# Optimization experiments

Measured on AMD Instinct MI355X. Metric: run time of the kernel, lower is better.

The kernel has to match this reference:

```python
import jax, jax.numpy as jnp
import numpy as np

N_NODES = 50000
N_RELS = 8
IN_DIM = 128
OUT_DIM = 128
N_EDGES = 800000


def setup_inputs() -> dict:
    key = jax.random.key(0)
    k1, k2, k3, k4 = jax.random.split(key, 4)
    src = jax.random.randint(k1, (N_EDGES,), 0, N_NODES, dtype=jnp.int64 if jax.config.jax_enable_x64 else jnp.int32)
    rel = jax.random.randint(k2, (N_EDGES,), 0, N_RELS, dtype=src.dtype)
    tgt = jax.random.randint(k3, (N_EDGES,), 0, N_NODES, dtype=src.dtype)
    triples = jnp.stack([src, rel, tgt], axis=1)  # (E, 3) like torch layout (s, r, t)
    features = jax.random.normal(k4, (N_NODES, IN_DIM), dtype=jnp.float32)
    weights = jax.random.normal(jax.random.fold_in(key, 1), (N_RELS, IN_DIM, OUT_DIM), dtype=jnp.float32) * (1.0 / np.sqrt(IN_DIM))
    bias = jnp.zeros((OUT_DIM,), dtype=jnp.float32)
    return {"triples": triples, "features": features, "weights": weights, "bias": bias}


def reference(triples, features, weights, bias):
    # RGCN-NC forward, horizontal stacking (featured mode):
    #   out[t] = sum_{(s,r,t) in E} (1/c_{t,r}) * features[s] @ W[r] + bias
    # where c_{t,r} = #edges sharing the same (relation, target) pair,
    # matching sum_sparse(..., row_normalisation=False) on the (n x r*n) adjacency.
    src, rel, tgt = triples[:, 0], triples[:, 1], triples[:, 2]
    n = features.shape[0]
    r = weights.shape[0]
    e = triples.shape[0]

    # per-(rel, tgt) edge counts -> 1/c normalization per edge
    key = rel * n + tgt  # column index of horizontally stacked adjacency
    counts = jax.ops.segment_sum(jnp.ones((e,), dtype=features.dtype), key, num_segments=r * n)
    vals = 1.0 / counts[key]  # (E,)

    # dense per-relation transform: H[r] = X @ W[r]   (r, n, out)
    h = jnp.einsum('ni,rio->rno', features, weights)

    # gather per-edge messages, scale, scatter-add into targets
    msgs = h[rel, src] * vals[:, None]  # (E, out)
    out = jax.ops.segment_sum(msgs, tgt, num_segments=n)  # (n, out)
    return out + bias
```

## Files before the change

### kernel.cpp

```cpp
#include <hip/hip_runtime.h>
#include <hip/hip_bf16.h>

#define N_NODES 50000
#define N_RELS 8
#define IN_DIM 128
#define OUT_DIM 128
#define N_EDGES 800000
#define NR (N_NODES * N_RELS)
#define KDIM (N_RELS * IN_DIM)
#define SCAN_ELEMS 2048
#define SCAN_NBLK ((NR + SCAN_ELEMS - 1) / SCAN_ELEMS)
#define M_PAD 50048
#define CNT_BLKS ((N_EDGES / 4 + 255) / 256)
#define CW_BLKS ((N_RELS * IN_DIM * OUT_DIM + 255) / 256)
#define FB_BLKS ((N_NODES * IN_DIM / 8 + 255) / 256)

typedef __attribute__((ext_vector_type(8))) short bf16x8;
typedef __attribute__((ext_vector_type(4))) float floatx4;
typedef __attribute__((ext_vector_type(4))) unsigned int uintx4;

__device__ inline unsigned short f2bf(float f) {
    unsigned u = __builtin_bit_cast(unsigned, f);
    u += 0x7fff + ((u >> 16) & 1);
    return (unsigned short)(u >> 16);
}
__device__ inline float bflo(unsigned u) {
    return __builtin_bit_cast(float, u << 16);
}
__device__ inline float bfhi(unsigned u) {
    return __builtin_bit_cast(float, u & 0xffff0000u);
}

__global__ void prep_kernel(const int* __restrict__ tri, const float* __restrict__ W,
                            const float* __restrict__ features,
                            int* __restrict__ cnt, unsigned short* __restrict__ Wtf,
                            unsigned short* __restrict__ featB) {
    const int b = blockIdx.x;
    if (b < CNT_BLKS) {
        int t = b * 256 + threadIdx.x;
        if (t >= N_EDGES / 4) return;
        const int4* tri4 = (const int4*)tri;
        int4 a = tri4[3 * t], v = tri4[3 * t + 1], c = tri4[3 * t + 2];
        atomicAdd(&cnt[a.z * N_RELS + a.y], 1);
        atomicAdd(&cnt[v.y * N_RELS + v.x], 1);
        atomicAdd(&cnt[c.x * N_RELS + v.w], 1);
        atomicAdd(&cnt[c.w * N_RELS + c.z], 1);
    } else if (b < CNT_BLKS + CW_BLKS) {
        int idx = (b - CNT_BLKS) * 256 + threadIdx.x;
        if (idx >= N_RELS * IN_DIM * OUT_DIM) return;
        int e  = idx & 7;
        int l  = (idx >> 3) & 63;
        int ks = (idx >> 9) & 31;
        int nt = idx >> 14;
        int o = nt * 16 + (l & 15);
        int k = ks * 32 + (l >> 4) * 8 + e;
        Wtf[idx] = f2bf(W[(k >> 7) * (IN_DIM * OUT_DIM) + (k & 127) * OUT_DIM + o]);
    } else {
        int t = (b - CNT_BLKS - CW_BLKS) * 256 + threadIdx.x;
        if (t >= N_NODES * IN_DIM / 8) return;
        const float4* f4 = (const float4*)features;
        float4 x = f4[2 * t], y = f4[2 * t + 1];
        uint4 o;
        o.x = (unsigned)f2bf(x.x) | ((unsigned)f2bf(x.y) << 16);
        o.y = (unsigned)f2bf(x.z) | ((unsigned)f2bf(x.w) << 16);
        o.z = (unsigned)f2bf(y.x) | ((unsigned)f2bf(y.y) << 16);
        o.w = (unsigned)f2bf(y.z) | ((unsigned)f2bf(y.w) << 16);
        ((uint4*)featB)[t] = o;
    }
}

__global__ void scan_part(const int* __restrict__ cnt, int* __restrict__ bsum) {
    __shared__ int s[256];
    int b = blockIdx.x, t = threadIdx.x;
    int base = b * SCAN_ELEMS + t * 8;
    int sum = 0;
#pragma unroll
    for (int k = 0; k < 8; ++k) {
        int i = base + k;
        sum += (i < NR) ? cnt[i] : 0;
    }
    s[t] = sum; __syncthreads();
    for (int off = 128; off > 0; off >>= 1) {
        if (t < off) s[t] += s[t + off];
        __syncthreads();
    }
    if (t == 0) bsum[b] = s[0];
}

__global__ __launch_bounds__(256) void scan_fused(
    const int* __restrict__ cnt, const int* __restrict__ bsum,
    int* __restrict__ segOff, int* __restrict__ cursor)
{
    __shared__ int s[256];
    __shared__ int sboff;
    const int b = blockIdx.x, t = threadIdx.x;

    int vb = (t < SCAN_NBLK) ? bsum[t] : 0;
    s[t] = vb; __syncthreads();
    for (int off = 1; off < 256; off <<= 1) {
        int x = (t >= off) ? s[t - off] : 0;
        __syncthreads();
        s[t] += x;
        __syncthreads();
    }
    if (t == 0) sboff = (b == 0) ? 0 : s[b - 1];
    __syncthreads();
    const int boff = sboff;

    const int base = b * SCAN_ELEMS + t * 8;
    int v[8]; int sum = 0;
#pragma unroll
    for (int k = 0; k < 8; ++k) {
        int i = base + k;
        v[k] = (i < NR) ? cnt[i] : 0;
        sum += v[k];
    }
    s[t] = sum; __syncthreads();
    for (int off = 1; off < 256; off <<= 1) {
        int x = (t >= off) ? s[t - off] : 0;
        __syncthreads();
        s[t] += x;
        __syncthreads();
    }
    int run = boff + s[t] - sum;
#pragma unroll
    for (int k = 0; k < 8; ++k) {
        int i = base + k;
        if (i < NR) { segOff[i] = run; cursor[i] = run; run += v[k]; }
    }
    if (b == 0 && t == 0) segOff[NR] = N_EDGES;
}

__global__ void scatter_kernel(const int* __restrict__ tri, int* __restrict__ cursor,
                               int* __restrict__ sortedSrc) {
    int e = blockIdx.x * 256 + threadIdx.x;
    if (e >= N_EDGES) return;
    int src = tri[3 * e];
    int rel = tri[3 * e + 1];
    int tgt = tri[3 * e + 2];
    int p = atomicAdd(&cursor[tgt * N_RELS + rel], 1);
    sortedSrc[p] = src;
}

__global__ __launch_bounds__(256) void agg_kernel(
    const int* __restrict__ sortedSrc, const int* __restrict__ segOff,
    const unsigned short* __restrict__ featB, unsigned short* __restrict__ aggG)
{
    const int wave = threadIdx.x >> 6, lane = threadIdx.x & 63;
    const int node = blockIdx.x * 4 + wave;
    const int q = lane >> 4, l16 = lane & 15;

    int bnd = 0;
    if (lane < 9) bnd = segOff[node * N_RELS + lane];
    int s[9];
#pragma unroll
    for (int i = 0; i < 9; ++i) s[i] = __shfl(bnd, i);

    const int e0 = s[0], eN = s[8];
    int srcw = 0;
    if (e0 + lane < eN) srcw = sortedSrc[e0 + lane];

    const unsigned short* fb = featB + 8 * l16;
    unsigned short* dst = aggG + (size_t)node * KDIM + 8 * l16;

#pragma unroll
    for (int p = 0; p < 2; ++p) {
        const int r = 4 * p + q;
        const int s0v = s[r], s1v = s[r + 1];
        const int len = s1v - s0v;
        int m0x = __shfl_xor(len, 16);
        int jm = (len > m0x) ? len : m0x;
        int m1x = __shfl_xor(jm, 32);
        const int jmax = (jm > m1x) ? jm : m1x;
        float a0 = 0.f, a1 = 0.f, a2 = 0.f, a3 = 0.f;
        float a4 = 0.f, a5 = 0.f, a6 = 0.f, a7 = 0.f;
        for (int j = 0; j < jmax; j += 2) {
            const int ea = s0v + j;
            const int ia = ea - e0;
            const int swina = __shfl(srcw, ia & 63);
            const int eb = ea + 1;
            const int ib = ia + 1;
            const int swinb = __shfl(srcw, ib & 63);
            const bool pa = j < len;
            const bool pb = j + 1 < len;
            int srca = 0, srcb = 0;
            if (pa) srca = (ia < 64) ? swina : sortedSrc[ea];
            if (pb) srcb = (ib < 64) ? swinb : sortedSrc[eb];
            uint4 ua = *(const uint4*)&fb[srca * IN_DIM];
            uint4 ub = *(const uint4*)&fb[srcb * IN_DIM];
            if (pa) {
                a0 += bflo(ua.x); a1 += bfhi(ua.x);
                a2 += bflo(ua.y); a3 += bfhi(ua.y);
                a4 += bflo(ua.z); a5 += bfhi(ua.z);
                a6 += bflo(ua.w); a7 += bfhi(ua.w);
            }
            if (pb) {
                a0 += bflo(ub.x); a1 += bfhi(ub.x);
                a2 += bflo(ub.y); a3 += bfhi(ub.y);
                a4 += bflo(ub.z); a5 += bfhi(ub.z);
                a6 += bflo(ub.w); a7 += bfhi(ub.w);
            }
        }
        const float inv = (len > 0) ? 1.0f / (float)len : 0.0f;
        uintx4 pk;
        pk[0] = (unsigned)f2bf(a0 * inv) | ((unsigned)f2bf(a1 * inv) << 16);
        pk[1] = (unsigned)f2bf(a2 * inv) | ((unsigned)f2bf(a3 * inv) << 16);
        pk[2] = (unsigned)f2bf(a4 * inv) | ((unsigned)f2bf(a5 * inv) << 16);
        pk[3] = (unsigned)f2bf(a6 * inv) | ((unsigned)f2bf(a7 * inv) << 16);
        __builtin_nontemporal_store(pk, (uintx4*)&dst[r * IN_DIM]);
    }
}

__global__ __launch_bounds__(256) void gemm_kernel(
    const unsigned short* __restrict__ aggG,
    const unsigned short* __restrict__ Wtf,
    const float* __restrict__ bias,
    float* __restrict__ out)
{
    __shared__ unsigned short Abuf[64 * 128];
    const int tid = threadIdx.x;
    const int wave = tid >> 6, lane = tid & 63;
    const int qk = lane >> 4, ln16 = lane & 15;
    const int m0 = blockIdx.x * 64;
    const int wm = wave & 1, wn = wave >> 1;

    floatx4 acc[2][4];
#pragma unroll
    for (int st = 0; st < 2; ++st)
#pragma unroll
        for (int nt = 0; nt < 4; ++nt) acc[st][nt] = (floatx4){0.f, 0.f, 0.f, 0.f};

    const int l4 = lane >> 4, l15 = lane & 15;

    for (int c = 0; c < 8; ++c) {
        __syncthreads();
#pragma unroll
        for (int i = 0; i < 4; ++i) {
            const int row = wave * 16 + i * 4 + l4;
            const int unit = l15 ^ (row & 15);
            const unsigned short* g =
                aggG + (size_t)(m0 + row) * KDIM + c * 128 + unit * 8;
            __builtin_amdgcn_global_load_lds(
                (const __attribute__((address_space(1))) unsigned int*)g,
                (__attribute__((address_space(3))) unsigned int*)&Abuf[(wave * 16 + i * 4) * 128],
                16, 0, 0);
        }
        __syncthreads();

#pragma unroll
        for (int ksl = 0; ksl < 4; ++ksl) {
            const int ks = c * 4 + ksl;
            bf16x8 a[2];
#pragma unroll
            for (int st = 0; st < 2; ++st) {
                const int r = wm * 32 + st * 16 + ln16;
                const int u = (ksl * 4 + qk) ^ (r & 15);
                a[st] = *(const bf16x8*)&Abuf[r * 128 + u * 8];
            }
#pragma unroll
            for (int nt = 0; nt < 4; ++nt) {
                const int ntg = wn * 4 + nt;
                bf16x8 b = *(const bf16x8*)&Wtf[(size_t)((ntg * 32 + ks) * 64 + lane) * 8];
                acc[0][nt] = __builtin_amdgcn_mfma_f32_16x16x32_bf16(a[0], b, acc[0][nt], 0, 0, 0);
                acc[1][nt] = __builtin_amdgcn_mfma_f32_16x16x32_bf16(a[1], b, acc[1][nt], 0, 0, 0);
            }
        }
    }

#pragma unroll
    for (int nt = 0; nt < 4; ++nt) {
        const int o = (wn * 4 + nt) * 16 + ln16;
        const float bv = bias[o];
#pragma unroll
        for (int st = 0; st < 2; ++st)
#pragma unroll
            for (int j = 0; j < 4; ++j) {
                const int t = m0 + wm * 32 + st * 16 + qk * 4 + j;
                if (t < N_NODES) out[(size_t)t * OUT_DIM + o] = acc[st][nt][j] + bv;
            }
    }
}

extern "C" void kernel_launch(void* const* d_in, const int* in_sizes, int n_in,
                              void* d_out, int out_size, void* d_ws, size_t ws_size,
                              hipStream_t stream)
{
    const int*   tri      = (const int*)d_in[0];
    const float* features = (const float*)d_in[1];
    const float* W        = (const float*)d_in[2];
    const float* bias     = (const float*)d_in[3];
    float* out = (float*)d_out;

    char* ws = (char*)d_ws;
    unsigned short* Wtf = (unsigned short*)ws; ws += (size_t)OUT_DIM * KDIM * 2;
    int* cnt       = (int*)ws; ws += (size_t)NR * 4;
    int* segOff    = (int*)ws; ws += (size_t)(NR + 4) * 4;
    int* cursor    = (int*)ws; ws += (size_t)NR * 4;
    int* bsum      = (int*)ws; ws += (size_t)SCAN_NBLK * 4;
    int* sortedSrc = (int*)ws; ws += (size_t)N_EDGES * 4;
    unsigned short* featB = (unsigned short*)ws; ws += (size_t)N_NODES * IN_DIM * 2;
    unsigned short* aggG  = (unsigned short*)ws; ws += (size_t)M_PAD * KDIM * 2;
    (void)ws_size; (void)in_sizes; (void)n_in; (void)out_size;

    hipMemsetAsync(cnt, 0, NR * sizeof(int), stream);
    prep_kernel<<<CNT_BLKS + CW_BLKS + FB_BLKS, 256, 0, stream>>>(tri, W, features, cnt, Wtf, featB);
    scan_part<<<SCAN_NBLK, 256, 0, stream>>>(cnt, bsum);
    scan_fused<<<SCAN_NBLK, 256, 0, stream>>>(cnt, bsum, segOff, cursor);
    scatter_kernel<<<(N_EDGES + 255) / 256, 256, 0, stream>>>(tri, cursor, sortedSrc);
    agg_kernel<<<N_NODES / 4, 256, 0, stream>>>(sortedSrc, segOff, featB, aggG);
    gemm_kernel<<<M_PAD / 64, 256, 0, stream>>>(aggG, Wtf, bias, out);
}
```

Measured before the change: 266.8 us.

## Fuse neighbor aggregation into GEMM via shared-memory A tile

Merges the aggregation and GEMM kernels into one kernel. Each 512-thread block aggregates 64 nodes' per-relation means into a 64KB LDS tile in two halves of four relations each, then runs MFMA over that tile. This removes the ~100MB bf16 aggG round trip through global memory and one kernel launch. The costs are a large LDS footprint that limits occupancy, serialized gather-then-compute phases within a block with barriers between them, and a tail block that skips nodes past the end. Output stores also become nontemporal.

Result: faster. 259.7 us (-2.7%).

```diff
diff --git a/kernel.cpp b/kernel.cpp
--- a/kernel.cpp
+++ b/kernel.cpp
@@ -10,7 +10,7 @@
 #define KDIM (N_RELS * IN_DIM)
 #define SCAN_ELEMS 2048
 #define SCAN_NBLK ((NR + SCAN_ELEMS - 1) / SCAN_ELEMS)
-#define M_PAD 50048
+#define FUSE_BLKS 782
 #define CNT_BLKS ((N_EDGES / 4 + 255) / 256)
 #define CW_BLKS ((N_RELS * IN_DIM * OUT_DIM + 255) / 256)
 #define FB_BLKS ((N_NODES * IN_DIM / 8 + 255) / 256)
@@ -142,141 +142,123 @@
     sortedSrc[p] = src;
 }
 
-__global__ __launch_bounds__(256) void agg_kernel(
+__global__ __launch_bounds__(512, 4) void fused_kernel(
     const int* __restrict__ sortedSrc, const int* __restrict__ segOff,
-    const unsigned short* __restrict__ featB, unsigned short* __restrict__ aggG)
-{
-    const int wave = threadIdx.x >> 6, lane = threadIdx.x & 63;
-    const int node = blockIdx.x * 4 + wave;
-    const int q = lane >> 4, l16 = lane & 15;
-
-    int bnd = 0;
-    if (lane < 9) bnd = segOff[node * N_RELS + lane];
-    int s[9];
-#pragma unroll
-    for (int i = 0; i < 9; ++i) s[i] = __shfl(bnd, i);
-
-    const int e0 = s[0], eN = s[8];
-    int srcw = 0;
-    if (e0 + lane < eN) srcw = sortedSrc[e0 + lane];
-
-    const unsigned short* fb = featB + 8 * l16;
-    unsigned short* dst = aggG + (size_t)node * KDIM + 8 * l16;
-
-#pragma unroll
-    for (int p = 0; p < 2; ++p) {
-        const int r = 4 * p + q;
-        const int s0v = s[r], s1v = s[r + 1];
-        const int len = s1v - s0v;
-        int m0x = __shfl_xor(len, 16);
-        int jm = (len > m0x) ? len : m0x;
-        int m1x = __shfl_xor(jm, 32);
-        const int jmax = (jm > m1x) ? jm : m1x;
-        float a0 = 0.f, a1 = 0.f, a2 = 0.f, a3 = 0.f;
-        float a4 = 0.f, a5 = 0.f, a6 = 0.f, a7 = 0.f;
-        for (int j = 0; j < jmax; j += 2) {
-            const int ea = s0v + j;
-            const int ia = ea - e0;
-            const int swina = __shfl(srcw, ia & 63);
-            const int eb = ea + 1;
-            const int ib = ia + 1;
-            const int swinb = __shfl(srcw, ib & 63);
-            const bool pa = j < len;
-            const bool pb = j + 1 < len;
-            int srca = 0, srcb = 0;
-            if (pa) srca = (ia < 64) ? swina : sortedSrc[ea];
-            if (pb) srcb = (ib < 64) ? swinb : sortedSrc[eb];
-            uint4 ua = *(const uint4*)&fb[srca * IN_DIM];
-            uint4 ub = *(const uint4*)&fb[srcb * IN_DIM];
-            if (pa) {
-                a0 += bflo(ua.x); a1 += bfhi(ua.x);
-                a2 += bflo(ua.y); a3 += bfhi(ua.y);
-                a4 += bflo(ua.z); a5 += bfhi(ua.z);
-                a6 += bflo(ua.w); a7 += bfhi(ua.w);
-            }
-            if (pb) {
-                a0 += bflo(ub.x); a1 += bfhi(ub.x);
-                a2 += bflo(ub.y); a3 += bfhi(ub.y);
-                a4 += bflo(ub.z); a5 += bfhi(ub.z);
-                a6 += bflo(ub.w); a7 += bfhi(ub.w);
-            }
-        }
-        const float inv = (len > 0) ? 1.0f / (float)len : 0.0f;
-        uintx4 pk;
-        pk[0] = (unsigned)f2bf(a0 * inv) | ((unsigned)f2bf(a1 * inv) << 16);
-        pk[1] = (unsigned)f2bf(a2 * inv) | ((unsigned)f2bf(a3 * inv) << 16);
-        pk[2] = (unsigned)f2bf(a4 * inv) | ((unsigned)f2bf(a5 * inv) << 16);
-        pk[3] = (unsigned)f2bf(a6 * inv) | ((unsigned)f2bf(a7 * inv) << 16);
-        __builtin_nontemporal_store(pk, (uintx4*)&dst[r * IN_DIM]);
-    }
-}
-
-__global__ __launch_bounds__(256) void gemm_kernel(
-    const unsigned short* __restrict__ aggG,
+    const unsigned short* __restrict__ featB,
     const unsigned short* __restrict__ Wtf,
     const float* __restrict__ bias,
     float* __restrict__ out)
 {
-    __shared__ unsigned short Abuf[64 * 128];
+    __shared__ unsigned short Atile[64 * 512];
     const int tid = threadIdx.x;
     const int wave = tid >> 6, lane = tid & 63;
-    const int qk = lane >> 4, ln16 = lane & 15;
+    const int q = lane >> 4, l16 = lane & 15;
     const int m0 = blockIdx.x * 64;
     const int wm = wave & 1, wn = wave >> 1;
 
-    floatx4 acc[2][4];
+    floatx4 acc[2][2];
 #pragma unroll
     for (int st = 0; st < 2; ++st)
 #pragma unroll
-        for (int nt = 0; nt < 4; ++nt) acc[st][nt] = (floatx4){0.f, 0.f, 0.f, 0.f};
-
-    const int l4 = lane >> 4, l15 = lane & 15;
-
-    for (int c = 0; c < 8; ++c) {
-        __syncthreads();
-#pragma unroll
-        for (int i = 0; i < 4; ++i) {
-            const int row = wave * 16 + i * 4 + l4;
-            const int unit = l15 ^ (row & 15);
-            const unsigned short* g =
-                aggG + (size_t)(m0 + row) * KDIM + c * 128 + unit * 8;
-            __builtin_amdgcn_global_load_lds(
-                (const __attribute__((address_space(1))) unsigned int*)g,
-                (__attribute__((address_space(3))) unsigned int*)&Abuf[(wave * 16 + i * 4) * 128],
-                16, 0, 0);
+        for (int nt = 0; nt < 2; ++nt) acc[st][nt] = (floatx4){0.f, 0.f, 0.f, 0.f};
+
+    const unsigned short* fb = featB + 8 * l16;
+
+#pragma unroll
+    for (int p = 0; p < 2; ++p) {
+        for (int i = 0; i < 8; ++i) {
+            const int nl = wave * 8 + i;
+            const int node = m0 + nl;
+            if (node < N_NODES) {
+                int bnd = 0;
+                if (lane < 5) bnd = segOff[node * N_RELS + 4 * p + lane];
+                int sg[5];
+#pragma unroll
+                for (int k = 0; k < 5; ++k) sg[k] = __shfl(bnd, k);
+
+                const int e0 = sg[0], eN = sg[4];
+                int srcw = 0;
+                if (e0 + lane < eN) srcw = sortedSrc[e0 + lane];
+
+                const int s0v = sg[q], s1v = sg[q + 1];
+                const int len = s1v - s0v;
+                int m0x = __shfl_xor(len, 16);
+                int jm = (len > m0x) ? len : m0x;
+                int m1x = __shfl_xor(jm, 32);
+                const int jmax = (jm > m1x) ? jm : m1x;
+                float a0 = 0.f, a1 = 0.f, a2 = 0.f, a3 = 0.f;
+                float a4 = 0.f, a5 = 0.f, a6 = 0.f, a7 = 0.f;
+                for (int j = 0; j < jmax; j += 2) {
+                    const int ea = s0v + j;
+                    const int ia = ea - e0;
+                    const int swina = __shfl(srcw, ia & 63);
+                    const int ib = ia + 1;
+                    const int swinb = __shfl(srcw, ib & 63);
+                    const bool pa = j < len;
+                    const bool pb = j + 1 < len;
+                    int srca = 0, srcb = 0;
+                    if (pa) srca = (ia < 64) ? swina : sortedSrc[ea];
+                    if (pb) srcb = (ib < 64) ? swinb : sortedSrc[ea + 1];
+                    uint4 ua = *(const uint4*)&fb[srca * IN_DIM];
+                    uint4 ub = *(const uint4*)&fb[srcb * IN_DIM];
+                    if (pa) {
+                        a0 += bflo(ua.x); a1 += bfhi(ua.x);
+                        a2 += bflo(ua.y); a3 += bfhi(ua.y);
+                        a4 += bflo(ua.z); a5 += bfhi(ua.z);
+                        a6 += bflo(ua.w); a7 += bfhi(ua.w);
+                    }
+                    if (pb) {
+                        a0 += bflo(ub.x); a1 += bfhi(ub.x);
+                        a2 += bflo(ub.y); a3 += bfhi(ub.y);
+                        a4 += bflo(ub.z); a5 += bfhi(ub.z);
+                        a6 += bflo(ub.w); a7 += bfhi(ub.w);
+                    }
+                }
+                const float inv = (len > 0) ? 1.0f / (float)len : 0.0f;
+                uintx4 pk;
+                pk[0] = (unsigned)f2bf(a0 * inv) | ((unsigned)f2bf(a1 * inv) << 16);
+                pk[1] = (unsigned)f2bf(a2 * inv) | ((unsigned)f2bf(a3 * inv) << 16);
+                pk[2] = (unsigned)f2bf(a4 * inv) | ((unsigned)f2bf(a5 * inv) << 16);
+                pk[3] = (unsigned)f2bf(a6 * inv) | ((unsigned)f2bf(a7 * inv) << 16);
+                const int us = (q * 16 + l16) ^ (nl & 15);
+                *(uintx4*)&Atile[(nl * 64 + us) * 8] = pk;
+            }
         }
         __syncthreads();
 
 #pragma unroll
-        for (int ksl = 0; ksl < 4; ++ksl) {
-            const int ks = c * 4 + ksl;
+        for (int ksl = 0; ksl < 16; ++ksl) {
+            const int ks = p * 16 + ksl;
             bf16x8 a[2];
 #pragma unroll
             for (int st = 0; st < 2; ++st) {
-                const int r = wm * 32 + st * 16 + ln16;
-                const int u = (ksl * 4 + qk) ^ (r & 15);
-                a[st] = *(const bf16x8*)&Abuf[r * 128 + u * 8];
-            }
-#pragma unroll
-            for (int nt = 0; nt < 4; ++nt) {
-                const int ntg = wn * 4 + nt;
+                const int r = wm * 32 + st * 16 + l16;
+                const int us = (ksl * 4 + q) ^ (r & 15);
+                a[st] = *(const bf16x8*)&Atile[(r * 64 + us) * 8];
+            }
+#pragma unroll
+            for (int nt = 0; nt < 2; ++nt) {
+                const int ntg = wn * 2 + nt;
                 bf16x8 b = *(const bf16x8*)&Wtf[(size_t)((ntg * 32 + ks) * 64 + lane) * 8];
                 acc[0][nt] = __builtin_amdgcn_mfma_f32_16x16x32_bf16(a[0], b, acc[0][nt], 0, 0, 0);
                 acc[1][nt] = __builtin_amdgcn_mfma_f32_16x16x32_bf16(a[1], b, acc[1][nt], 0, 0, 0);
             }
         }
-    }
-
-#pragma unroll
-    for (int nt = 0; nt < 4; ++nt) {
-        const int o = (wn * 4 + nt) * 16 + ln16;
+        __syncthreads();
+    }
+
+#pragma unroll
+    for (int nt = 0; nt < 2; ++nt) {
+        const int o = (wn * 2 + nt) * 16 + l16;
         const float bv = bias[o];
 #pragma unroll
         for (int st = 0; st < 2; ++st)
 #pragma unroll
             for (int j = 0; j < 4; ++j) {
-                const int t = m0 + wm * 32 + st * 16 + qk * 4 + j;
-                if (t < N_NODES) out[(size_t)t * OUT_DIM + o] = acc[st][nt][j] + bv;
+                const int t = m0 + wm * 32 + st * 16 + q * 4 + j;
+                if (t < N_NODES)
+                    __builtin_nontemporal_store(acc[st][nt][j] + bv,
+                                                &out[(size_t)t * OUT_DIM + o]);
             }
     }
 }
@@ -299,7 +281,6 @@
     int* bsum      = (int*)ws; ws += (size_t)SCAN_NBLK * 4;
     int* sortedSrc = (int*)ws; ws += (size_t)N_EDGES * 4;
     unsigned short* featB = (unsigned short*)ws; ws += (size_t)N_NODES * IN_DIM * 2;
-    unsigned short* aggG  = (unsigned short*)ws; ws += (size_t)M_PAD * KDIM * 2;
     (void)ws_size; (void)in_sizes; (void)n_in; (void)out_size;
 
     hipMemsetAsync(cnt, 0, NR * sizeof(int), stream);
@@ -307,6 +288,5 @@
     scan_part<<<SCAN_NBLK, 256, 0, stream>>>(cnt, bsum);
     scan_fused<<<SCAN_NBLK, 256, 0, stream>>>(cnt, bsum, segOff, cursor);
     scatter_kernel<<<(N_EDGES + 255) / 256, 256, 0, stream>>>(tri, cursor, sortedSrc);
-    agg_kernel<<<N_NODES / 4, 256, 0, stream>>>(sortedSrc, segOff, featB, aggG);
-    gemm_kernel<<<M_PAD / 64, 256, 0, stream>>>(aggG, Wtf, bias, out);
-}
+    fused_kernel<<<FUSE_BLKS, 512, 0, stream>>>(sortedSrc, segOff, featB, Wtf, bias, out);
+}
```
